# Kernel optimization log

Hardware: AMD Instinct MI355X
Metric: run time of the kernel (lower is better)

The kernel has to match this reference:

```python
import jax, jax.numpy as jnp
import numpy as np

B, S, E, P, K, H = 32, 512, 1024, 256, 3, 8
KERNELS = 4  # conv repeated KERNELS times then averaged -> identical to a single conv


def setup_inputs() -> dict:
    key = jax.random.key(0)
    ks = jax.random.split(key, 8)
    sc = 0.02
    x = jax.random.normal(ks[0], (B, S, E), jnp.float32)
    # lengths must satisfy 3 <= l <= S-1 so slice [1:l+1] and conv length l-2 are valid
    seq_length = jax.random.randint(ks[1], (B,), 16, S - 1)
    proj_w = jax.random.normal(ks[2], (E, P), jnp.float32) * sc
    proj_b = jnp.zeros((P,), jnp.float32)
    conv_w = jax.random.normal(ks[3], (P, P, K), jnp.float32) * sc  # (out, in, width)
    conv_b = jnp.zeros((P,), jnp.float32)
    attn_w = jax.random.normal(ks[4], (P, H * S), jnp.float32) * sc
    attn_b = jnp.zeros((H * S,), jnp.float32)
    c1_w = jax.random.normal(ks[5], (P, P // 2), jnp.float32) * sc
    c1_b = jnp.zeros((P // 2,), jnp.float32)
    c2_w = jax.random.normal(ks[6], (P // 2, 2), jnp.float32) * sc
    c2_b = jnp.zeros((2,), jnp.float32)
    return dict(x=x, seq_length=seq_length, proj_w=proj_w, proj_b=proj_b,
                conv_w=conv_w, conv_b=conv_b, attn_w=attn_w, attn_b=attn_b,
                c1_w=c1_w, c1_b=c1_b, c2_w=c2_w, c2_b=c2_b)


def _forward(x, seq_length, proj_w, proj_b, conv_w, conv_b, attn_w, attn_b,
             c1_w, c1_b, c2_w, c2_b):
    # projection: (B,S,E) -> (B,S,P)
    proj = jnp.einsum('bse,ep->bsp', x, proj_w) + proj_b
    proj_pc = jnp.transpose(proj, (0, 2, 1))  # (B,P,S)
    # original convs each sample over slice [1:l+1]; conv is local, so conv the
    # full slice [1:] once and mask invalid tail positions per sample.
    conv = jax.lax.conv_general_dilated(
        proj_pc[:, :, 1:], conv_w, window_strides=(1,), padding='VALID',
        dimension_numbers=('NCH', 'OIH', 'NCH'))  # (B,P,S-K)
    conv = jax.nn.relu(conv + conv_b[None, :, None])
    # sum of KERNELS identical relu(conv) outputs divided by KERNELS == conv (identity)
    m = S - K  # conv output length over slice [1:]
    l = seq_length[:, None]  # (B,1)
    valid = jnp.arange(m)[None, :] < (l - (K - 1))  # output j valid iff j < l-2
    conv = jnp.where(valid[:, None, :], conv, 0.0)
    # pad: position 0 zero, conv outputs at 1..l-2, zeros after -> (B,P,S)
    rep_conv = jnp.zeros((B, P, S), conv.dtype).at[:, :, 1:1 + m].set(conv)
    rep_conv = jnp.transpose(rep_conv, (0, 2, 1))  # (B,S,P)
    # attention: logits (B,S,H*S), softmax over the FULL H*S axis (original dim=1)
    logits = jnp.einsum('bsp,pk->bsk', rep_conv, attn_w) + attn_b
    attn = jax.nn.softmax(logits, axis=-1).reshape(B, S, H, S)
    # per sample: mean over heads, sum over query rows -> weights over key pos q
    w = attn.sum(axis=(1, 2)) / H  # (B,S)
    rep_attn = jnp.einsum('bq,bqp->bp', w, rep_conv)  # (B,P)
    h = jnp.einsum('bp,ph->bh', rep_attn, c1_w) + c1_b
    h = jnp.where(h > 0, h, 0.01 * h)  # LeakyReLU(0.01)
    cls = jnp.einsum('bh,hc->bc', h, c2_w) + c2_b
    return jax.nn.softmax(cls, axis=-1)


def reference(x, seq_length, proj_w, proj_b, conv_w, conv_b, attn_w, attn_b,
              c1_w, c1_b, c2_w, c2_b):
    probs = _forward(x, seq_length, proj_w, proj_b, conv_w, conv_b,
                     attn_w, attn_b, c1_w, c1_b, c2_w, c2_b)
    return probs, jnp.argmax(probs, axis=1)
```

## Files before the change

### kernel.cpp

```cpp
#include <hip/hip_runtime.h>
#include <hip/hip_fp8.h>

#define B_ 32
#define S_ 512
#define E_ 1024
#define P_ 256
#define HH 8

typedef __attribute__((ext_vector_type(8))) short bf16x8;
typedef __attribute__((ext_vector_type(8))) unsigned short us8;
typedef __attribute__((ext_vector_type(4))) unsigned short us4;
typedef __attribute__((ext_vector_type(16))) float f32x16;
typedef __attribute__((ext_vector_type(4))) float f32x4;
typedef __attribute__((ext_vector_type(8))) unsigned char u8x8;

#define SA 8.0f
#define SB 16.0f
#define SINV (1.0f / 128.0f)
#define LOG2E 1.44269504088896f
#define SINV2 (SINV * LOG2E)

static __device__ __forceinline__ unsigned short f2bf(float f) {
  union { float f; unsigned int u; } v;
  v.f = f;
  unsigned int r = (v.u + 0x7FFFu + ((v.u >> 16) & 1u)) >> 16;
  return (unsigned short)r;
}
static __device__ __forceinline__ float bf2f(unsigned short u) {
  union { unsigned int u; float f; } v;
  v.u = ((unsigned int)u) << 16;
  return v.f;
}
static __device__ __forceinline__ unsigned char f2fp8(float f) {
  return (unsigned char)__hip_cvt_float_to_fp8(f, __HIP_SATFINITE, __HIP_E4M3);
}

__global__ __launch_bounds__(256) void k_prep(const float* __restrict__ pw,
                                              const float* __restrict__ cw,
                                              const float* __restrict__ aw,
                                              unsigned short* __restrict__ pwB,
                                              unsigned short* __restrict__ wtB,
                                              unsigned char* __restrict__ awB8,
                                              float* __restrict__ zbase) {
  int bid = blockIdx.x;
  int t = threadIdx.x;
  if (bid < 160) {
    zbase[bid * 256 + t] = 0.f;
    return;
  }
  bid -= 160;
  if (bid < 128) {
    int g = bid >> 4, kc = (bid & 15) * 4 + (t >> 6);
    int l = t & 63;
    int n = g * 32 + (l & 31);
    int kbase = kc * 16 + (l >> 5) * 8;
    us8 v;
#pragma unroll
    for (int j = 0; j < 8; j++) v[j] = f2bf(pw[(size_t)(kbase + j) * P_ + n]);
    *(us8*)(pwB + ((size_t)g * 64 + kc) * 512 + l * 8) = v;
    return;
  }
  bid -= 128;
  if (bid < 96) {
    int g = bid / 12, kidx = (bid % 12) * 4 + (t >> 6);
    int l = t & 63;
    int o = g * 32 + (l & 31);
    int xb = kidx * 16 + (l >> 5) * 8;
    us8 v;
#pragma unroll
    for (int j = 0; j < 8; j++) {
      int x = xb + j;
      int k = x >> 8, i = x & 255;
      v[j] = f2bf(cw[(size_t)o * 768 + i * 3 + k]);
    }
    *(us8*)(wtB + ((size_t)g * 48 + kidx) * 512 + l * 8) = v;
    return;
  }
  bid -= 96;
  {
    int g = bid >> 1, ks = (bid & 1) * 4 + (t >> 6);
    int l = t & 63;
    int j0 = g * 16 + (l & 15);
    int kbase = ks * 32 + (l >> 4) * 8;
    u8x8 v;
#pragma unroll
    for (int j = 0; j < 8; j++) v[j] = f2fp8(aw[(size_t)(kbase + j) * 4096 + j0] * SB);
    *(u8x8*)(awB8 + ((size_t)g * 8 + ks) * 512 + l * 8) = v;
  }
}

__global__ __launch_bounds__(256) void k_swz8(const unsigned short* __restrict__ src,
                                              unsigned char* __restrict__ dst) {
  int g = blockIdx.x, ks = blockIdx.y * 4 + (threadIdx.x >> 6);
  int l = threadIdx.x & 63;
  us8 v = *(const us8*)(src + (size_t)(g * 16 + (l & 15)) * 256 + ks * 32 + (l >> 4) * 8);
  u8x8 o;
#pragma unroll
  for (int j = 0; j < 8; j++) o[j] = f2fp8(bf2f(v[j]) * SA);
  *(u8x8*)(dst + ((size_t)g * 8 + ks) * 512 + l * 8) = o;
}

__global__ __launch_bounds__(512) void k_proj_mfma(const float* __restrict__ x,
                                                   const unsigned short* __restrict__ pwB,
                                                   const float* __restrict__ pb,
                                                   unsigned short* __restrict__ proj16) {
  __shared__ unsigned short As[16 * 64 * 8];
  const int m0 = blockIdx.x * 64;
  const int t = threadIdx.x;
  const int w = t >> 6, lane = t & 63, ln31 = lane & 31, kh = lane >> 5;
  const int c0 = w * 32;

  f32x16 acc0, acc1;
#pragma unroll
  for (int r = 0; r < 16; r++) { acc0[r] = 0.f; acc1[r] = 0.f; }

  const unsigned short* bp = pwB + (size_t)w * 64 * 512 + lane * 8;

  for (int kc = 0; kc < E_; kc += 128) {
#pragma unroll
    for (int i = 0; i < 4; i++) {
      int c = t + i * 512;
      int row = c >> 5, pos = c & 31;
      float4 v = *(const float4*)(x + (size_t)(m0 + row) * E_ + kc + pos * 4);
      us4 h;
      h[0] = f2bf(v.x); h[1] = f2bf(v.y); h[2] = f2bf(v.z); h[3] = f2bf(v.w);
      *(us4*)&As[((pos >> 1) * 64 + row) * 8 + (pos & 1) * 4] = h;
    }
    __syncthreads();
    const int kcs = kc >> 4;
#pragma unroll
    for (int kk = 0; kk < 8; kk++) {
      bf16x8 a0 = *(const bf16x8*)&As[((2 * kk + kh) * 64 + ln31) * 8];
      bf16x8 a1 = *(const bf16x8*)&As[((2 * kk + kh) * 64 + 32 + ln31) * 8];
      bf16x8 b  = *(const bf16x8*)(bp + (size_t)(kcs + kk) * 512);
      acc0 = __builtin_amdgcn_mfma_f32_32x32x16_bf16(a0, b, acc0, 0, 0, 0);
      acc1 = __builtin_amdgcn_mfma_f32_32x32x16_bf16(a1, b, acc1, 0, 0, 0);
    }
    __syncthreads();
  }
  float pbv = pb[c0 + ln31];
#pragma unroll
  for (int r = 0; r < 16; r++) {
    int rl = (r & 3) + 8 * (r >> 2) + 4 * kh;
    proj16[(size_t)(m0 + rl) * P_ + c0 + ln31]      = f2bf(acc0[r] + pbv);
    proj16[(size_t)(m0 + 32 + rl) * P_ + c0 + ln31] = f2bf(acc1[r] + pbv);
  }
}

__global__ __launch_bounds__(512) void k_conv_mfma(const unsigned short* __restrict__ proj16,
                                                   const unsigned short* __restrict__ wtB,
                                                   const float* __restrict__ cb,
                                                   const int* __restrict__ seq,
                                                   unsigned short* __restrict__ rep16) {
  __shared__ unsigned short As[32 * 66 * 8];
  const int m0 = blockIdx.x * 64;
  const int bb = m0 >> 9, s0 = m0 & 511;
  const int t = threadIdx.x;
  const int w = t >> 6, lane = t & 63, ln31 = lane & 31, kh = lane >> 5;
  const int c0 = w * 32;

#pragma unroll
  for (int i = 0; i < 5; i++) {
    int c = t + i * 512;
    if (c < 2112) {
      int row = c >> 5, kk2 = c & 31;
      us8 v = {0, 0, 0, 0, 0, 0, 0, 0};
      if (s0 + row <= 511)
        v = *(const us8*)(proj16 + (size_t)(bb * S_ + s0 + row) * P_ + kk2 * 8);
      *(us8*)&As[(kk2 * 66 + row) * 8] = v;
    }
  }
  __syncthreads();

  f32x16 acc0, acc1;
#pragma unroll
  for (int r = 0; r < 16; r++) { acc0[r] = 0.f; acc1[r] = 0.f; }

  const unsigned short* bbase = wtB + (size_t)w * 48 * 512 + lane * 8;

#pragma unroll
  for (int k = 0; k < 3; k++) {
#pragma unroll
    for (int kk = 0; kk < 16; kk++) {
      bf16x8 a0 = *(const bf16x8*)&As[((2 * kk + kh) * 66 + k + ln31) * 8];
      bf16x8 a1 = *(const bf16x8*)&As[((2 * kk + kh) * 66 + k + 32 + ln31) * 8];
      bf16x8 b  = *(const bf16x8*)(bbase + (size_t)(k * 16 + kk) * 512);
      acc0 = __builtin_amdgcn_mfma_f32_32x32x16_bf16(a0, b, acc0, 0, 0, 0);
      acc1 = __builtin_amdgcn_mfma_f32_32x32x16_bf16(a1, b, acc1, 0, 0, 0);
    }
  }

  int l = seq[bb];
  float cbv = cb[c0 + ln31];
#pragma unroll
  for (int r = 0; r < 16; r++) {
    int rl = (r & 3) + 8 * (r >> 2) + 4 * kh;
    int s_a = s0 + rl, s_b = s0 + 32 + rl;
    float ma = (s_a >= 1 && s_a <= 509 && s_a < l - 1) ? 1.f : 0.f;
    float mb = (s_b >= 1 && s_b <= 509 && s_b < l - 1) ? 1.f : 0.f;
    rep16[(size_t)(m0 + rl) * P_ + c0 + ln31]      = f2bf(fmaxf(acc0[r] + cbv, 0.f) * ma);
    rep16[(size_t)(m0 + 32 + rl) * P_ + c0 + ln31] = f2bf(fmaxf(acc1[r] + cbv, 0.f) * mb);
  }
}

__global__ __launch_bounds__(256) void k_attn_mfma(const unsigned char* __restrict__ repF8,
                                                   const unsigned char* __restrict__ awB8,
                                                   const float* __restrict__ ab,
                                                   unsigned short* __restrict__ E16,
                                                   float* __restrict__ Z) {
  __shared__ __align__(16) unsigned char As8[16384];
  const int m0 = blockIdx.x * 64;
  const int q0 = blockIdx.y * 128;
  const int t = threadIdx.x;
  const int w = t >> 6, lane = t & 63;
  const int ln15 = lane & 15, l4 = lane >> 4;

  {
    const float4* src = (const float4*)(repF8 + (size_t)m0 * 256);
    float4* dst = (float4*)As8;
#pragma unroll
    for (int i = 0; i < 4; i++) dst[t + i * 256] = src[t + i * 256];
  }
  __syncthreads();

  const int qg = (q0 >> 5) + w;

  f32x4 ef[8];
#pragma unroll
  for (int i = 0; i < 8; i++) ef[i] = (f32x4){0.f, 0.f, 0.f, 0.f};

#pragma unroll 1
  for (int h = 0; h < HH; h++) {
    unsigned oz = 0;
    asm volatile("" : "+v"(oz));
    const unsigned char* bh = awB8 + (size_t)(h * 32 + qg * 2) * 8 * 512 + lane * 8;
    f32x4 acc[8];
#pragma unroll
    for (int i = 0; i < 8; i++) acc[i] = (f32x4){0.f, 0.f, 0.f, 0.f};
#pragma unroll
    for (int ks = 0; ks < 8; ks++) {
      long b0 = *(const long*)(bh + (size_t)ks * 512);
      long b1 = *(const long*)(bh + (size_t)(8 + ks) * 512);
#pragma unroll
      for (int rt = 0; rt < 4; rt++) {
        long a = *(const long*)&As8[(rt * 8 + ks) * 512 + lane * 8 + oz];
        acc[rt * 2 + 0] = __builtin_amdgcn_mfma_f32_16x16x32_fp8_fp8(a, b0, acc[rt * 2 + 0], 0, 0, 0);
        acc[rt * 2 + 1] = __builtin_amdgcn_mfma_f32_16x16x32_fp8_fp8(a, b1, acc[rt * 2 + 1], 0, 0, 0);
      }
    }
    float bias0 = ab[h * 512 + qg * 32 + ln15] * LOG2E;
    float bias1 = ab[h * 512 + qg * 32 + 16 + ln15] * LOG2E;
#pragma unroll
    for (int rt = 0; rt < 4; rt++)
#pragma unroll
      for (int r = 0; r < 4; r++) {
        ef[rt * 2 + 0][r] += __builtin_amdgcn_exp2f(acc[rt * 2 + 0][r] * SINV2 + bias0);
        ef[rt * 2 + 1][r] += __builtin_amdgcn_exp2f(acc[rt * 2 + 1][r] * SINV2 + bias1);
      }
  }

#pragma unroll
  for (int rt = 0; rt < 4; rt++)
#pragma unroll
    for (int r = 0; r < 4; r++) {
      int row = m0 + rt * 16 + l4 * 4 + r;
      E16[(size_t)row * 512 + qg * 32 + ln15]      = f2bf(ef[rt * 2 + 0][r]);
      E16[(size_t)row * 512 + qg * 32 + 16 + ln15] = f2bf(ef[rt * 2 + 1][r]);
    }

#pragma unroll
  for (int rt = 0; rt < 4; rt++)
#pragma unroll
    for (int r = 0; r < 4; r++) {
      float z = ef[rt * 2 + 0][r] + ef[rt * 2 + 1][r];
#pragma unroll
      for (int st = 8; st >= 1; st >>= 1) z += __shfl_xor(z, st, 64);
      if (ln15 == 0) atomicAdd(&Z[m0 + rt * 16 + l4 * 4 + r], z);
    }
}

__global__ __launch_bounds__(512) void k_w(const unsigned short* __restrict__ E16,
                                           const float* __restrict__ Z,
                                           float* __restrict__ wB) {
  __shared__ float rZ[64];
  int b = blockIdx.x, c = blockIdx.y, t = threadIdx.x;
  int s0 = c * 64;
  if (t < 64) rZ[t] = 1.0f / Z[b * 512 + s0 + t];
  __syncthreads();
  float acc = 0.f;
#pragma unroll 8
  for (int s = 0; s < 64; s++)
    acc += bf2f(E16[(size_t)(b * 512 + s0 + s) * 512 + t]) * rZ[s];
  atomicAdd(&wB[b * 512 + t], acc * (1.0f / HH));
}

__global__ __launch_bounds__(256) void k_final_a(const unsigned short* __restrict__ rep16,
                                                 const float* __restrict__ wB,
                                                 float* __restrict__ repA) {
  __shared__ float wS[64];
  int b = blockIdx.x, qc = blockIdx.y, t = threadIdx.x;
  if (t < 64) wS[t] = wB[b * 512 + qc * 64 + t];
  __syncthreads();
  int p0 = (t & 63) * 4, qo = t >> 6;
  float a0 = 0.f, a1 = 0.f, a2 = 0.f, a3 = 0.f;
  for (int q = qo; q < 64; q += 4) {
    us4 v = *(const us4*)(rep16 + (size_t)(b * 512 + qc * 64 + q) * 256 + p0);
    float wq = wS[q];
    a0 += wq * bf2f(v[0]); a1 += wq * bf2f(v[1]);
    a2 += wq * bf2f(v[2]); a3 += wq * bf2f(v[3]);
  }
  atomicAdd(&repA[b * 256 + p0 + 0], a0);
  atomicAdd(&repA[b * 256 + p0 + 1], a1);
  atomicAdd(&repA[b * 256 + p0 + 2], a2);
  atomicAdd(&repA[b * 256 + p0 + 3], a3);
}

__global__ __launch_bounds__(128) void k_final_b(const float* __restrict__ repA,
                                                 const float* __restrict__ c1w,
                                                 const float* __restrict__ c1b,
                                                 const float* __restrict__ c2w,
                                                 const float* __restrict__ c2b,
                                                 float* __restrict__ out) {
  __shared__ float hS[128];
  __shared__ float clsS[2];
  int b = blockIdx.x, t = threadIdx.x;
  float acc = c1b[t];
  for (int p = 0; p < 256; p++) acc += repA[b * 256 + p] * c1w[p * 128 + t];
  hS[t] = acc > 0.f ? acc : 0.01f * acc;
  __syncthreads();
  if (t < 2) {
    float a2 = c2b[t];
    for (int j = 0; j < 128; j++) a2 += hS[j] * c2w[j * 2 + t];
    clsS[t] = a2;
  }
  __syncthreads();
  if (t == 0) {
    float c0 = clsS[0], c1 = clsS[1];
    float m = fmaxf(c0, c1);
    float e0 = __expf(c0 - m), e1 = __expf(c1 - m);
    float inv = 1.0f / (e0 + e1);
    float p0 = e0 * inv, p1 = e1 * inv;
    out[b * 2 + 0] = p0;
    out[b * 2 + 1] = p1;
    out[B_ * 2 + b] = (p1 > p0) ? 1.0f : 0.0f;
  }
}

extern "C" void kernel_launch(void* const* d_in, const int* in_sizes, int n_in,
                              void* d_out, int out_size, void* d_ws, size_t ws_size,
                              hipStream_t stream) {
  const float* x   = (const float*)d_in[0];
  const int*   seq = (const int*)d_in[1];
  const float* pw  = (const float*)d_in[2];
  const float* pb  = (const float*)d_in[3];
  const float* cw  = (const float*)d_in[4];
  const float* cb  = (const float*)d_in[5];
  const float* aw  = (const float*)d_in[6];
  const float* ab  = (const float*)d_in[7];
  const float* c1w = (const float*)d_in[8];
  const float* c1b = (const float*)d_in[9];
  const float* c2w = (const float*)d_in[10];
  const float* c2b = (const float*)d_in[11];
  float* out = (float*)d_out;

  char* ws = (char*)d_ws;
  unsigned short* proj16 = (unsigned short*)(ws);
  unsigned short* E16    = (unsigned short*)(ws);
  unsigned short* rep16  = (unsigned short*)(ws + (size_t)16777216);
  unsigned char*  repF8  = (unsigned char*)(ws + (size_t)25165824);
  unsigned char*  awB8   = (unsigned char*)(ws + (size_t)29360128);
  unsigned short* pwB    = (unsigned short*)(ws + (size_t)30408704);
  unsigned short* wtB    = (unsigned short*)(ws + (size_t)30932992);
  float*          Z      = (float*)(ws + (size_t)31326208);
  float*          wB     = (float*)(ws + (size_t)31391744);
  float*          repA   = (float*)(ws + (size_t)31457280);

  k_prep<<<896, 256, 0, stream>>>(pw, cw, aw, pwB, wtB, awB8, Z);
  k_proj_mfma<<<256, 512, 0, stream>>>(x, pwB, pb, proj16);
  k_conv_mfma<<<256, 512, 0, stream>>>(proj16, wtB, cb, seq, rep16);
  k_swz8<<<dim3(1024, 2), 256, 0, stream>>>(rep16, repF8);
  k_attn_mfma<<<dim3(256, 4), 256, 0, stream>>>(repF8, awB8, ab, E16, Z);
  k_w<<<dim3(32, 8), 512, 0, stream>>>(E16, Z, wB);
  k_final_a<<<dim3(32, 8), 256, 0, stream>>>(rep16, wB, repA);
  k_final_b<<<32, 128, 0, stream>>>(repA, c1w, c1b, c2w, c2b, out);
}
```

Before: 213.9 us.

## Fuse fp8 swizzle into conv, double-buffer proj loads, split attn accumulators

The conv kernel now writes the fp8 swizzled copy of its output directly, which removes the separate swizzle launch and its reread of the bf16 buffer. The projection kernel double-buffers its shared-memory A tile and prefetches the next x chunk into registers while the MFMAs run, to hide global load latency. The attention kernel processes the two 16-column halves one after the other with four accumulators instead of eight, to lower register pressure. The costs are scattered byte-sized fp8 stores from conv and twice the shared memory in proj.

```diff
diff --git a/kernel.cpp b/kernel.cpp
--- a/kernel.cpp
+++ b/kernel.cpp
@@ -89,55 +89,75 @@
   }
 }
 
-__global__ __launch_bounds__(256) void k_swz8(const unsigned short* __restrict__ src,
-                                              unsigned char* __restrict__ dst) {
-  int g = blockIdx.x, ks = blockIdx.y * 4 + (threadIdx.x >> 6);
-  int l = threadIdx.x & 63;
-  us8 v = *(const us8*)(src + (size_t)(g * 16 + (l & 15)) * 256 + ks * 32 + (l >> 4) * 8);
-  u8x8 o;
-#pragma unroll
-  for (int j = 0; j < 8; j++) o[j] = f2fp8(bf2f(v[j]) * SA);
-  *(u8x8*)(dst + ((size_t)g * 8 + ks) * 512 + l * 8) = o;
-}
-
 __global__ __launch_bounds__(512) void k_proj_mfma(const float* __restrict__ x,
                                                    const unsigned short* __restrict__ pwB,
                                                    const float* __restrict__ pb,
                                                    unsigned short* __restrict__ proj16) {
-  __shared__ unsigned short As[16 * 64 * 8];
+  __shared__ unsigned short As[2][16 * 64 * 8];
   const int m0 = blockIdx.x * 64;
   const int t = threadIdx.x;
   const int w = t >> 6, lane = t & 63, ln31 = lane & 31, kh = lane >> 5;
   const int c0 = w * 32;
+  const int rbase = t >> 5, pos = t & 31;
 
   f32x16 acc0, acc1;
 #pragma unroll
   for (int r = 0; r < 16; r++) { acc0[r] = 0.f; acc1[r] = 0.f; }
 
   const unsigned short* bp = pwB + (size_t)w * 64 * 512 + lane * 8;
-
-  for (int kc = 0; kc < E_; kc += 128) {
-#pragma unroll
-    for (int i = 0; i < 4; i++) {
-      int c = t + i * 512;
-      int row = c >> 5, pos = c & 31;
-      float4 v = *(const float4*)(x + (size_t)(m0 + row) * E_ + kc + pos * 4);
-      us4 h;
-      h[0] = f2bf(v.x); h[1] = f2bf(v.y); h[2] = f2bf(v.z); h[3] = f2bf(v.w);
-      *(us4*)&As[((pos >> 1) * 64 + row) * 8 + (pos & 1) * 4] = h;
-    }
-    __syncthreads();
-    const int kcs = kc >> 4;
+  const float* xbase = x + (size_t)(m0 + rbase) * E_ + pos * 4;
+
+  float4 v0, v1, v2, v3;
+  v0 = *(const float4*)(xbase);
+  v1 = *(const float4*)(xbase + 16 * E_);
+  v2 = *(const float4*)(xbase + 32 * E_);
+  v3 = *(const float4*)(xbase + 48 * E_);
+  {
+    us4 h;
+    h[0] = f2bf(v0.x); h[1] = f2bf(v0.y); h[2] = f2bf(v0.z); h[3] = f2bf(v0.w);
+    *(us4*)&As[0][((pos >> 1) * 64 + rbase) * 8 + (pos & 1) * 4] = h;
+    h[0] = f2bf(v1.x); h[1] = f2bf(v1.y); h[2] = f2bf(v1.z); h[3] = f2bf(v1.w);
+    *(us4*)&As[0][((pos >> 1) * 64 + rbase + 16) * 8 + (pos & 1) * 4] = h;
+    h[0] = f2bf(v2.x); h[1] = f2bf(v2.y); h[2] = f2bf(v2.z); h[3] = f2bf(v2.w);
+    *(us4*)&As[0][((pos >> 1) * 64 + rbase + 32) * 8 + (pos & 1) * 4] = h;
+    h[0] = f2bf(v3.x); h[1] = f2bf(v3.y); h[2] = f2bf(v3.z); h[3] = f2bf(v3.w);
+    *(us4*)&As[0][((pos >> 1) * 64 + rbase + 48) * 8 + (pos & 1) * 4] = h;
+  }
+  __syncthreads();
+
+  for (int k8 = 0; k8 < 8; k8++) {
+    const int cur = k8 & 1;
+    if (k8 < 7) {
+      const float* xs = xbase + (k8 + 1) * 128;
+      v0 = *(const float4*)(xs);
+      v1 = *(const float4*)(xs + 16 * E_);
+      v2 = *(const float4*)(xs + 32 * E_);
+      v3 = *(const float4*)(xs + 48 * E_);
+    }
+    const int kcs = k8 * 8;
 #pragma unroll
     for (int kk = 0; kk < 8; kk++) {
-      bf16x8 a0 = *(const bf16x8*)&As[((2 * kk + kh) * 64 + ln31) * 8];
-      bf16x8 a1 = *(const bf16x8*)&As[((2 * kk + kh) * 64 + 32 + ln31) * 8];
+      bf16x8 a0 = *(const bf16x8*)&As[cur][((2 * kk + kh) * 64 + ln31) * 8];
+      bf16x8 a1 = *(const bf16x8*)&As[cur][((2 * kk + kh) * 64 + 32 + ln31) * 8];
       bf16x8 b  = *(const bf16x8*)(bp + (size_t)(kcs + kk) * 512);
       acc0 = __builtin_amdgcn_mfma_f32_32x32x16_bf16(a0, b, acc0, 0, 0, 0);
       acc1 = __builtin_amdgcn_mfma_f32_32x32x16_bf16(a1, b, acc1, 0, 0, 0);
     }
+    if (k8 < 7) {
+      const int nxt = cur ^ 1;
+      us4 h;
+      h[0] = f2bf(v0.x); h[1] = f2bf(v0.y); h[2] = f2bf(v0.z); h[3] = f2bf(v0.w);
+      *(us4*)&As[nxt][((pos >> 1) * 64 + rbase) * 8 + (pos & 1) * 4] = h;
+      h[0] = f2bf(v1.x); h[1] = f2bf(v1.y); h[2] = f2bf(v1.z); h[3] = f2bf(v1.w);
+      *(us4*)&As[nxt][((pos >> 1) * 64 + rbase + 16) * 8 + (pos & 1) * 4] = h;
+      h[0] = f2bf(v2.x); h[1] = f2bf(v2.y); h[2] = f2bf(v2.z); h[3] = f2bf(v2.w);
+      *(us4*)&As[nxt][((pos >> 1) * 64 + rbase + 32) * 8 + (pos & 1) * 4] = h;
+      h[0] = f2bf(v3.x); h[1] = f2bf(v3.y); h[2] = f2bf(v3.z); h[3] = f2bf(v3.w);
+      *(us4*)&As[nxt][((pos >> 1) * 64 + rbase + 48) * 8 + (pos & 1) * 4] = h;
+    }
     __syncthreads();
   }
+
   float pbv = pb[c0 + ln31];
 #pragma unroll
   for (int r = 0; r < 16; r++) {
@@ -151,7 +171,8 @@
                                                    const unsigned short* __restrict__ wtB,
                                                    const float* __restrict__ cb,
                                                    const int* __restrict__ seq,
-                                                   unsigned short* __restrict__ rep16) {
+                                                   unsigned short* __restrict__ rep16,
+                                                   unsigned char* __restrict__ repF8) {
   __shared__ unsigned short As[32 * 66 * 8];
   const int m0 = blockIdx.x * 64;
   const int bb = m0 >> 9, s0 = m0 & 511;
@@ -192,14 +213,20 @@
 
   int l = seq[bb];
   float cbv = cb[c0 + ln31];
+  const int g0 = m0 >> 4;
+  const int colpart = ((ln31 >> 3) & 3) * 128 + (ln31 & 7);
 #pragma unroll
   for (int r = 0; r < 16; r++) {
     int rl = (r & 3) + 8 * (r >> 2) + 4 * kh;
     int s_a = s0 + rl, s_b = s0 + 32 + rl;
     float ma = (s_a >= 1 && s_a <= 509 && s_a < l - 1) ? 1.f : 0.f;
     float mb = (s_b >= 1 && s_b <= 509 && s_b < l - 1) ? 1.f : 0.f;
-    rep16[(size_t)(m0 + rl) * P_ + c0 + ln31]      = f2bf(fmaxf(acc0[r] + cbv, 0.f) * ma);
-    rep16[(size_t)(m0 + 32 + rl) * P_ + c0 + ln31] = f2bf(fmaxf(acc1[r] + cbv, 0.f) * mb);
+    float va = fmaxf(acc0[r] + cbv, 0.f) * ma;
+    float vb = fmaxf(acc1[r] + cbv, 0.f) * mb;
+    rep16[(size_t)(m0 + rl) * P_ + c0 + ln31]      = f2bf(va);
+    rep16[(size_t)(m0 + 32 + rl) * P_ + c0 + ln31] = f2bf(vb);
+    repF8[((size_t)((g0 + (rl >> 4)) * 8 + w)) * 512 + (rl & 15) * 8 + colpart]     = f2fp8(va * SA);
+    repF8[((size_t)((g0 + 2 + (rl >> 4)) * 8 + w)) * 512 + (rl & 15) * 8 + colpart] = f2fp8(vb * SA);
   }
 }
 
@@ -231,32 +258,30 @@
 
 #pragma unroll 1
   for (int h = 0; h < HH; h++) {
-    unsigned oz = 0;
-    asm volatile("" : "+v"(oz));
     const unsigned char* bh = awB8 + (size_t)(h * 32 + qg * 2) * 8 * 512 + lane * 8;
-    f32x4 acc[8];
-#pragma unroll
-    for (int i = 0; i < 8; i++) acc[i] = (f32x4){0.f, 0.f, 0.f, 0.f};
-#pragma unroll
-    for (int ks = 0; ks < 8; ks++) {
-      long b0 = *(const long*)(bh + (size_t)ks * 512);
-      long b1 = *(const long*)(bh + (size_t)(8 + ks) * 512);
-#pragma unroll
-      for (int rt = 0; rt < 4; rt++) {
-        long a = *(const long*)&As8[(rt * 8 + ks) * 512 + lane * 8 + oz];
-        acc[rt * 2 + 0] = __builtin_amdgcn_mfma_f32_16x16x32_fp8_fp8(a, b0, acc[rt * 2 + 0], 0, 0, 0);
-        acc[rt * 2 + 1] = __builtin_amdgcn_mfma_f32_16x16x32_fp8_fp8(a, b1, acc[rt * 2 + 1], 0, 0, 0);
+#pragma unroll
+    for (int qt = 0; qt < 2; qt++) {
+      unsigned oz = 0;
+      asm volatile("" : "+v"(oz));
+      f32x4 acc[4];
+#pragma unroll
+      for (int i = 0; i < 4; i++) acc[i] = (f32x4){0.f, 0.f, 0.f, 0.f};
+#pragma unroll
+      for (int ks = 0; ks < 8; ks++) {
+        long bv = *(const long*)(bh + (size_t)(qt * 8 + ks) * 512);
+#pragma unroll
+        for (int rt = 0; rt < 4; rt++) {
+          long a = *(const long*)&As8[(rt * 8 + ks) * 512 + lane * 8 + oz];
+          acc[rt] = __builtin_amdgcn_mfma_f32_16x16x32_fp8_fp8(a, bv, acc[rt], 0, 0, 0);
+        }
       }
-    }
-    float bias0 = ab[h * 512 + qg * 32 + ln15] * LOG2E;
-    float bias1 = ab[h * 512 + qg * 32 + 16 + ln15] * LOG2E;
-#pragma unroll
-    for (int rt = 0; rt < 4; rt++)
-#pragma unroll
-      for (int r = 0; r < 4; r++) {
-        ef[rt * 2 + 0][r] += __builtin_amdgcn_exp2f(acc[rt * 2 + 0][r] * SINV2 + bias0);
-        ef[rt * 2 + 1][r] += __builtin_amdgcn_exp2f(acc[rt * 2 + 1][r] * SINV2 + bias1);
-      }
+      float bias = ab[h * 512 + qg * 32 + qt * 16 + ln15] * LOG2E;
+#pragma unroll
+      for (int rt = 0; rt < 4; rt++)
+#pragma unroll
+        for (int r = 0; r < 4; r++)
+          ef[rt * 2 + qt][r] += __builtin_amdgcn_exp2f(acc[rt][r] * SINV2 + bias);
+    }
   }
 
 #pragma unroll
@@ -377,8 +402,7 @@
 
   k_prep<<<896, 256, 0, stream>>>(pw, cw, aw, pwB, wtB, awB8, Z);
   k_proj_mfma<<<256, 512, 0, stream>>>(x, pwB, pb, proj16);
-  k_conv_mfma<<<256, 512, 0, stream>>>(proj16, wtB, cb, seq, rep16);
-  k_swz8<<<dim3(1024, 2), 256, 0, stream>>>(rep16, repF8);
+  k_conv_mfma<<<256, 512, 0, stream>>>(proj16, wtB, cb, seq, rep16, repF8);
   k_attn_mfma<<<dim3(256, 4), 256, 0, stream>>>(repF8, awB8, ab, E16, Z);
   k_w<<<dim3(32, 8), 512, 0, stream>>>(E16, Z, wB);
   k_final_a<<<dim3(32, 8), 256, 0, stream>>>(rep16, wB, repA);
```

Result: slower. 238.1 us (+11.4%).
